# Performance work log

Measured on AMD Instinct MI355X. Metric: run time of the kernel, lower is better.

The kernel has to match this reference:

```python
import jax, jax.numpy as jnp
import numpy as np


def median_pool8(x):
    # x: (N, 1, H0, W0); 8x8 non-overlapping blocks, lower median (torch.median semantics)
    N, C, H0, W0 = x.shape
    H, W = H0 // 8, W0 // 8
    blocks = x.reshape(N, C, H, 8, W, 8).transpose(0, 1, 2, 4, 3, 5).reshape(N, C, H, W, 64)
    return jnp.sort(blocks, axis=-1)[..., (64 - 1) // 2]


def prelu(x, a):
    return jnp.where(x >= 0, x, a * x)


def setup_inputs() -> dict:
    key = jax.random.key(0)
    ks = jax.random.split(key, 12)
    N, C, H, W = 8, 128, 45, 60
    s = 0.05
    return {
        "cnn_encoder_output": jax.random.normal(ks[0], (N, C, H, W), jnp.float32),
        "original_input": jax.random.uniform(ks[1], (N, 4, H * 8, W * 8), jnp.float32),
        "xy": jax.random.normal(ks[2], (N, 2, H * 8, W * 8), jnp.float32),
        # g MLP: two Linear(128,128) + PReLU (single alpha each)
        "g_w0": jax.random.normal(ks[3], (C, C), jnp.float32) * s,
        "g_b0": jnp.zeros((C,), jnp.float32),
        "g_a0": jnp.full((1,), 0.25, jnp.float32),
        "g_w1": jax.random.normal(ks[4], (C, C), jnp.float32) * s,
        "g_b1": jnp.zeros((C,), jnp.float32),
        "g_a1": jnp.full((1,), 0.25, jnp.float32),
        # q update: Linear(256,128) + PReLU
        "q_w": jax.random.normal(ks[5], (C, 2 * C), jnp.float32) * s,
        "q_b": jnp.zeros((C,), jnp.float32),
        "q_a": jnp.full((1,), 0.25, jnp.float32),
        # output conv: Conv2d(256, 128, 3, padding=1)
        "conv_w": jax.random.normal(ks[6], (C, 2 * C, 3, 3), jnp.float32) * s,
        "conv_b": jnp.zeros((C,), jnp.float32),
        "gnn_iterations": 2,
        "k": 16,
        "use_half_precision": 0,
    }


def reference(cnn_encoder_output, original_input, xy,
              g_w0, g_b0, g_a0, g_w1, g_b1, g_a1,
              q_w, q_b, q_a, conv_w, conv_b,
              gnn_iterations, k, use_half_precision):
    N, C, H, W = cnn_encoder_output.shape
    HW = H * W

    # 3D projection: median-pooled x, y, depth -> (N, HW, 3)
    depth = median_pool8(original_input[:, 3:4])
    xc = median_pool8(xy[:, 0:1])
    yc = median_pool8(xy[:, 1:2])
    proj = jnp.concatenate([xc, yc, depth], axis=1).reshape(N, 3, HW).transpose(0, 2, 1)

    # batched KNN: D_ij = sqrt(|pi|^2 + |pj|^2 - 2 pi.pj), k smallest per row
    sq = jnp.sum(proj * proj, axis=-1)                        # (N, HW)
    r = jnp.einsum('nic,njc->nij', proj, proj)                # (N, HW, HW)
    D = jnp.sqrt(jnp.maximum(sq[:, :, None] + sq[:, None, :] - 2.0 * r, 0.0))
    _, knn = jax.lax.top_k(-D, k)                             # (N, HW, K) indices

    h = cnn_encoder_output.transpose(0, 2, 3, 1).reshape(N, HW, C)
    g_params = [(g_w0, g_b0, g_a0), (g_w1, g_b1, g_a1)]

    for _ in range(gnn_iterations):
        # gather neighbor features: (N, HW, K, C)
        nf = jax.vmap(lambda hn, kn: hn[kn])(h, knn)
        for w, b, a in g_params:
            nf = prelu(nf @ w.T + b, a)
        m = jnp.mean(nf, axis=2)                              # (N, HW, C)
        h = prelu(jnp.concatenate([h, m], axis=-1) @ q_w.T + q_b, q_a)

    h_img = h.reshape(N, H, W, C).transpose(0, 3, 1, 2)
    inp = jnp.concatenate([cnn_encoder_output, h_img], axis=1)  # (N, 2C, H, W)
    out = jax.lax.conv_general_dilated(
        inp, conv_w, window_strides=(1, 1), padding=((1, 1), (1, 1)),
        dimension_numbers=('NCHW', 'OIHW', 'NCHW')) + conv_b[None, :, None, None]
    return out
```

## Files before the change

### kernel.cpp

```cpp
#include <hip/hip_runtime.h>
#include <cfloat>
#include <cmath>

#define NB 8
#define CC 128
#define HH 45
#define WW 60
#define HWP 2700
#define KNN 16
#define H0 360
#define W0 480
#define NT 43
#define MROWS 21600

typedef __bf16 bf16_8 __attribute__((ext_vector_type(8)));
typedef __bf16 bf16_4 __attribute__((ext_vector_type(4)));
typedef float  f32x4  __attribute__((ext_vector_type(4)));

template <int K>
__device__ __forceinline__ void wfrag_body(const float* __restrict__ Wt,
                                           __bf16* __restrict__ wf, int bx, int tid) {
    int t = bx * 256 + tid;
    int j = t & 7;
    int lane = (t >> 3) & 63;
    int nt = (t >> 9) & 7;
    int kc = t >> 12;
    int oc = nt * 16 + (lane & 15);
    int k = kc * 32 + (lane >> 4) * 8 + j;
    wf[t] = (__bf16)Wt[(size_t)oc * K + k];
}

__global__ void __launch_bounds__(256) setup_all(
    const float* __restrict__ cnn, const float* __restrict__ xy,
    const float* __restrict__ orig,
    const float* __restrict__ g_w0, const float* __restrict__ g_w1,
    const float* __restrict__ q_w, const float* __restrict__ conv_w,
    __bf16* __restrict__ cnn_b, __bf16* __restrict__ pad_in,
    float* __restrict__ proj,
    __bf16* __restrict__ g0f, __bf16* __restrict__ g1f,
    __bf16* __restrict__ qf, __bf16* __restrict__ w_frag) {
    int bx = blockIdx.x;
    int tid = threadIdx.x;
    if (bx < 2720) {
        __shared__ float tile[32][33];
        int n = bx / 340;
        int r2 = bx % 340;
        int c0 = (r2 / 85) * 32;
        int p0 = (r2 % 85) * 32;
        int tx = tid & 31, ty = tid >> 5;
        #pragma unroll
        for (int r = 0; r < 32; r += 8) {
            int c = c0 + ty + r, p = p0 + tx;
            tile[ty + r][tx] = (p < HWP) ? cnn[((size_t)n * CC + c) * HWP + p] : 0.f;
        }
        __syncthreads();
        #pragma unroll
        for (int r = 0; r < 32; r += 8) {
            int p = p0 + ty + r, c = c0 + tx;
            if (p < HWP) {
                __bf16 bv = (__bf16)tile[tx][ty + r];
                cnn_b[((size_t)n * HWP + p) * 128 + c] = bv;
                int y = p / WW, x = p % WW;
                pad_in[(((size_t)n * 47 + y + 1) * 68 + (x + 1)) * 256 + c] = bv;
            }
        }
    } else if (bx < 2720 + 16200) {
        int w = (bx - 2720) * 4 + (tid >> 6);
        int lane = tid & 63;
        int n = w / (3 * HWP);
        int rem = w % (3 * HWP);
        int c = rem / HWP;
        int b = rem % HWP;
        const float* src = (c < 2) ? (xy + ((size_t)n * 2 + c) * H0 * W0)
                                   : (orig + ((size_t)n * 4 + 3) * H0 * W0);
        int by = b / WW, bxp = b % WW;
        int r = lane >> 3, col = lane & 7;
        float v = src[(by * 8 + r) * W0 + bxp * 8 + col];
        #pragma unroll
        for (int k = 2; k <= 64; k <<= 1) {
            #pragma unroll
            for (int j2 = k >> 1; j2 >= 1; j2 >>= 1) {
                float p = __shfl_xor(v, j2, 64);
                bool dir = (lane & k) == 0;
                bool low = (lane & j2) == 0;
                v = (dir == low) ? fminf(v, p) : fmaxf(v, p);
            }
        }
        if (lane == 31) proj[(size_t)c * (NB * HWP) + (size_t)n * HWP + b] = v;
    } else if (bx < 2720 + 16200 + 1408) {
        int pb = bx - (2720 + 16200);
        if (pb < 64)        wfrag_body<128>(g_w0, g0f, pb, tid);
        else if (pb < 128)  wfrag_body<128>(g_w1, g1f, pb - 64, tid);
        else if (pb < 256)  wfrag_body<256>(q_w, qf, pb - 128, tid);
        else {
            int t = (pb - 256) * 256 + tid;
            int j = t & 7;
            int lane = (t >> 3) & 63;
            int ntile = (t >> 9) & 7;
            int icc = (t >> 12) & 7;
            int tap = t >> 15;
            int oc = ntile * 16 + (lane & 15);
            int ic = icc * 32 + (lane >> 4) * 8 + j;
            w_frag[t] = (__bf16)conv_w[((size_t)oc * 256 + ic) * 9 + tap];
        }
    } else {
        int t = (bx - (2720 + 16200 + 1408)) * 256 + tid;
        int cg = t & 31;
        int s = t >> 5;
        int cell = s % 496;
        int n = s / 496;
        int y, x;
        if (cell < 136) { y = (cell < 68) ? 0 : 46; x = cell % 68; }
        else {
            int rem = cell - 136;
            y = 1 + rem / 8;
            int k = rem % 8;
            x = (k == 0) ? 0 : (60 + k);
        }
        bf16_8 z = {};
        *(bf16_8*)&pad_in[(((size_t)n * 47 + y) * 68 + x) * 256 + cg * 8] = z;
    }
}

__global__ void __launch_bounds__(512, 6) knn_kernel(const float* __restrict__ proj,
                                                     int* __restrict__ knn) {
#pragma clang fp contract(off)
    __shared__ float4 pts[HWP];
    __shared__ int sbufj[8][64];
    __shared__ int scnt[8];
    int n = blockIdx.y;
    const float* px = proj + (size_t)n * HWP;
    const float* py = proj + (size_t)NB * HWP + (size_t)n * HWP;
    const float* pz = proj + (size_t)2 * NB * HWP + (size_t)n * HWP;
    for (int t = threadIdx.x; t < HWP; t += 512) {
        float x = px[t], y = py[t], z = pz[t];
        float4 p;
        p.x = x; p.y = y; p.z = z;
        p.w = (x * x + y * y) + z * z;
        pts[t] = p;
    }
    __syncthreads();

    int wave = threadIdx.x >> 6;
    int lane = threadIdx.x & 63;
    int i = blockIdx.x * 8 + wave;
    if (i >= HWP) return;
    float4 pi = pts[i];
    float xi = pi.x, yi = pi.y, zi = pi.z, sqi = pi.w;

    unsigned int sdp[22];
    float mn = FLT_MAX;
    #pragma unroll
    for (int t = 0; t < NT; ++t) {
        int j = lane + t * 64;
        unsigned int u = 0xFFFFu;
        if (j < HWP) {
            float4 pj = pts[j];
            float r = fmaf(zi, pj.z, fmaf(yi, pj.y, xi * pj.x));
            float s = (sqi + pj.w) - 2.0f * r;
            mn = fminf(mn, s);
            float sc = fmaxf(s, 0.f);
            u = (__float_as_uint(sc) + 0xFFFFu) >> 16;
        }
        if (t & 1) sdp[t >> 1] |= (u << 16);
        else       sdp[t >> 1] = u;
    }

    float v = mn;
    #pragma unroll
    for (int k = 2; k <= 64; k <<= 1) {
        #pragma unroll
        for (int j2 = k >> 1; j2 >= 1; j2 >>= 1) {
            float p = __shfl_xor(v, j2, 64);
            bool dir = (lane & k) == 0;
            bool low = (lane & j2) == 0;
            v = (dir == low) ? fminf(v, p) : fmaxf(v, p);
        }
    }
    float M_s = __shfl(v, 15, 64);
    float M_test = (M_s > 0.f) ? (M_s * 1.0000005f + 1e-37f) : 0.0f;
    float M_t2 = M_test * 1.009f;
    unsigned int M16 = __float_as_uint(M_t2) >> 16;

    if (lane == 0) scnt[wave] = 0;
    #pragma unroll
    for (int t = 0; t < NT; ++t) {
        unsigned int u = (t & 1) ? (sdp[t >> 1] >> 16) : (sdp[t >> 1] & 0xFFFFu);
        if (u <= M16) {
            int slot = atomicAdd(&scnt[wave], 1);
            if (slot < 64) sbufj[wave][slot] = lane + t * 64;
        }
    }
    int cnt = scnt[wave];

    int myj = 0;
    if (cnt >= KNN && cnt <= 64) {
        unsigned long long key = ~0ull;
        if (lane < cnt) {
            int j = sbufj[wave][lane];
            float4 pj = pts[j];
            float r = fmaf(zi, pj.z, fmaf(yi, pj.y, xi * pj.x));
            float s = (sqi + pj.w) - 2.0f * r;
            float d = sqrtf(fmaxf(s, 0.f));
            key = ((unsigned long long)__float_as_uint(d) << 32) | (unsigned int)j;
        }
        #pragma unroll
        for (int k = 2; k <= 64; k <<= 1) {
            #pragma unroll
            for (int j2 = k >> 1; j2 >= 1; j2 >>= 1) {
                unsigned long long p = __shfl_xor(key, j2, 64);
                bool dir = (lane & k) == 0;
                bool low = (lane & j2) == 0;
                bool keepmin = (dir == low);
                bool pless = p < key;
                key = (pless == keepmin) ? p : key;
            }
        }
        myj = (int)(unsigned int)(key & 0xffffffffull);
    } else {
        float lastd = -FLT_MAX; int lastj = -1;
        #pragma unroll 1
        for (int r = 0; r < KNN; ++r) {
            float bd = FLT_MAX; int bj = 0x7fffffff;
            #pragma unroll 1
            for (int t = 0; t < NT; ++t) {
                int j = lane + t * 64;
                if (j < HWP) {
                    float4 pj = pts[j];
                    float rr = fmaf(zi, pj.z, fmaf(yi, pj.y, xi * pj.x));
                    float s = (sqi + pj.w) - 2.0f * rr;
                    float d = sqrtf(fmaxf(s, 0.f));
                    bool gt = (d > lastd) || (d == lastd && j > lastj);
                    bool lt = (d < bd) || (d == bd && j < bj);
                    if (gt && lt) { bd = d; bj = j; }
                }
            }
            float md = bd; int mj = bj;
            #pragma unroll
            for (int off = 32; off >= 1; off >>= 1) {
                float od = __shfl_xor(md, off, 64);
                int oj = __shfl_xor(mj, off, 64);
                if (od < md || (od == md && oj < mj)) { md = od; mj = oj; }
            }
            if (lane == r) myj = mj;
            lastd = md; lastj = mj;
        }
    }
    if (lane < KNN)
        knn[((size_t)n * HWP + i) * KNN + lane] = myj;
}

__device__ __forceinline__ void layer_b(
    const __bf16* __restrict__ src,
    const __bf16* __restrict__ wf,
    int wave, int lane, int kc_base, f32x4 acc[2][2]) {
    int quad = lane >> 4, lm = lane & 15;
    const bf16_8* wf8 = (const bf16_8*)wf;
    #pragma unroll
    for (int kc = 0; kc < 4; ++kc) {
        bf16_8 b[2], a[2];
        #pragma unroll
        for (int nt = 0; nt < 2; ++nt)
            b[nt] = *(const bf16_8*)&src[(nt * 16 + lm) * 136 + kc * 32 + quad * 8];
        #pragma unroll
        for (int mt = 0; mt < 2; ++mt)
            a[mt] = wf8[((size_t)(kc_base + kc) * 8 + (wave * 2 + mt)) * 64 + lane];
        #pragma unroll
        for (int mt = 0; mt < 2; ++mt)
            #pragma unroll
            for (int nt = 0; nt < 2; ++nt)
                acc[mt][nt] = __builtin_amdgcn_mfma_f32_16x16x32_bf16(
                    a[mt], b[nt], acc[mt][nt], 0, 0, 0);
    }
}

__global__ void __launch_bounds__(256) fused_g(
    const __bf16* __restrict__ Ain,
    const __bf16* __restrict__ w0f, const float* __restrict__ b0, const float* __restrict__ a0p,
    const __bf16* __restrict__ w1f, const float* __restrict__ b1, const float* __restrict__ a1p,
    __bf16* __restrict__ tgb) {
    __shared__ __bf16 albuf[32 * 136];
    __shared__ __bf16 inter[32 * 136];
    int bx = blockIdx.x;
    int nimg = bx & 7;
    int r0 = (bx >> 3) * 32;
    size_t base = (size_t)nimg * HWP;
    int tid = threadIdx.x;
    int wave = tid >> 6, lane = tid & 63;
    int quad = lane >> 4, lm = lane & 15;
    #pragma unroll
    for (int t = tid; t < 512; t += 256) {
        int row = t >> 4, c8 = (t & 15) * 8;
        int gr = r0 + row; if (gr >= HWP) gr = HWP - 1;
        *(bf16_8*)&albuf[row * 136 + c8] =
            *(const bf16_8*)&Ain[(base + gr) * 128 + c8];
    }
    __syncthreads();
    {
        f32x4 acc[2][2] = {};
        layer_b(albuf, w0f, wave, lane, 0, acc);
        float alpha = a0p[0];
        #pragma unroll
        for (int mt = 0; mt < 2; ++mt) {
            int oc0 = wave * 32 + mt * 16 + quad * 4;
            float4 bb = *(const float4*)&b0[oc0];
            float bv[4] = {bb.x, bb.y, bb.z, bb.w};
            #pragma unroll
            for (int nt = 0; nt < 2; ++nt) {
                bf16_4 o;
                #pragma unroll
                for (int reg = 0; reg < 4; ++reg) {
                    float vv = acc[mt][nt][reg] + bv[reg];
                    vv = (vv >= 0.f) ? vv : alpha * vv;
                    o[reg] = (__bf16)vv;
                }
                *(bf16_4*)&inter[(nt * 16 + lm) * 136 + oc0] = o;
            }
        }
    }
    __syncthreads();
    {
        f32x4 acc[2][2] = {};
        layer_b(inter, w1f, wave, lane, 0, acc);
        float alpha = a1p[0];
        #pragma unroll
        for (int mt = 0; mt < 2; ++mt) {
            int oc0 = wave * 32 + mt * 16 + quad * 4;
            float4 bb = *(const float4*)&b1[oc0];
            float bv[4] = {bb.x, bb.y, bb.z, bb.w};
            #pragma unroll
            for (int nt = 0; nt < 2; ++nt) {
                bf16_4 o;
                #pragma unroll
                for (int reg = 0; reg < 4; ++reg) {
                    float vv = acc[mt][nt][reg] + bv[reg];
                    vv = (vv >= 0.f) ? vv : alpha * vv;
                    o[reg] = (__bf16)vv;
                }
                int grow = r0 + nt * 16 + lm;
                if (grow < HWP)
                    *(bf16_4*)&tgb[(base + grow) * 128 + oc0] = o;
            }
        }
    }
}

__global__ void __launch_bounds__(256) fused_q(
    const __bf16* __restrict__ Ain, const __bf16* __restrict__ tgb,
    const int* __restrict__ knn_idx,
    const __bf16* __restrict__ qf, const float* __restrict__ qb,
    const float* __restrict__ qap,
    __bf16* __restrict__ out_lin, __bf16* __restrict__ pad_out, int mode) {
    __shared__ __bf16 hlds[32 * 136];
    __shared__ __bf16 mlds[32 * 136];
    int bx = blockIdx.x;
    int nimg = bx & 7;
    int r0 = (bx >> 3) * 32;
    size_t base = (size_t)nimg * HWP;
    int tid = threadIdx.x;
    int wave = tid >> 6, lane = tid & 63;
    int quad = lane >> 4, lm = lane & 15;
    #pragma unroll
    for (int t = tid; t < 512; t += 256) {
        int row = t >> 4, c8 = (t & 15) * 8;
        int gr = r0 + row; if (gr >= HWP) gr = HWP - 1;
        *(bf16_8*)&hlds[row * 136 + c8] =
            *(const bf16_8*)&Ain[(base + gr) * 128 + c8];
    }
    {
        int pix = tid >> 3;
        int oct0 = (tid & 7) * 2;
        int grow = r0 + pix; if (grow >= HWP) grow = HWP - 1;
        const int* kn = knn_idx + (base + grow) * KNN;
        const __bf16* tbase = tgb + base * 128;
        float a0[8] = {}, a1[8] = {};
        #pragma unroll
        for (int k = 0; k < KNN; ++k) {
            int j = kn[k];
            const __bf16* srcp = tbase + (size_t)j * 128 + oct0 * 8;
            bf16_8 v0 = *(const bf16_8*)srcp;
            bf16_8 v1 = *(const bf16_8*)(srcp + 8);
            #pragma unroll
            for (int e = 0; e < 8; ++e) { a0[e] += (float)v0[e]; a1[e] += (float)v1[e]; }
        }
        const float s = 1.f / 16.f;
        bf16_8 o0, o1;
        #pragma unroll
        for (int e = 0; e < 8; ++e) { o0[e] = (__bf16)(a0[e] * s); o1[e] = (__bf16)(a1[e] * s); }
        *(bf16_8*)&mlds[pix * 136 + oct0 * 8] = o0;
        *(bf16_8*)&mlds[pix * 136 + oct0 * 8 + 8] = o1;
    }
    __syncthreads();
    f32x4 acc[2][2] = {};
    layer_b(hlds, qf, wave, lane, 0, acc);
    layer_b(mlds, qf, wave, lane, 4, acc);
    float alpha = qap[0];
    #pragma unroll
    for (int mt = 0; mt < 2; ++mt) {
        int oc0 = wave * 32 + mt * 16 + quad * 4;
        float4 bb = *(const float4*)&qb[oc0];
        float bv[4] = {bb.x, bb.y, bb.z, bb.w};
        #pragma unroll
        for (int nt = 0; nt < 2; ++nt) {
            bf16_4 o;
            #pragma unroll
            for (int reg = 0; reg < 4; ++reg) {
                float vv = acc[mt][nt][reg] + bv[reg];
                vv = (vv >= 0.f) ? vv : alpha * vv;
                o[reg] = (__bf16)vv;
            }
            int grow = r0 + nt * 16 + lm;
            if (grow < HWP) {
                if (mode == 0) {
                    *(bf16_4*)&out_lin[(base + grow) * 128 + oc0] = o;
                } else {
                    int y = grow / WW, x = grow % WW;
                    *(bf16_4*)&pad_out[(((size_t)nimg * 47 + y + 1) * 68 + (x + 1)) * 256 + 128 + oc0] = o;
                }
            }
        }
    }
}

__global__ void __launch_bounds__(256) conv_mfma(
    const __bf16* __restrict__ pad_in,
    const __bf16* __restrict__ w_frag,
    const float* __restrict__ bias,
    float* __restrict__ out) {
    __shared__ __bf16 alds[3 * 66 * 72];
    int bx = blockIdx.x;
    int n = bx & 7;
    int rest = bx >> 3;
    int y = rest % HH;
    int oh = rest / HH;
    int tid = threadIdx.x;
    int wave = tid >> 6, lane = tid & 63;
    int wm = wave & 1, wq = wave >> 1;
    int quad = lane >> 4, lm = lane & 15;

    f32x4 acc[2][2] = {};
    const bf16_8* wf = (const bf16_8*)w_frag;

    for (int c64 = 0; c64 < 4; ++c64) {
        __syncthreads();
        for (int t = tid; t < 1584; t += 256) {
            int cq = t & 7;
            int xp = (t >> 3) % 66;
            int dy = (t >> 3) / 66;
            size_t src = (((size_t)n * 47 + (y + dy)) * 68 + xp) * 256 + c64 * 64 + cq * 8;
            *(bf16_8*)&alds[(dy * 66 + xp) * 72 + cq * 8] = *(const bf16_8*)&pad_in[src];
        }
        __syncthreads();
        #pragma unroll
        for (int tap = 0; tap < 9; ++tap) {
            int ky = tap / 3, kx = tap % 3;
            #pragma unroll
            for (int h = 0; h < 2; ++h) {
                int icc = c64 * 2 + h;
                bf16_8 b[2], a[2];
                #pragma unroll
                for (int nt = 0; nt < 2; ++nt)
                    b[nt] = wf[(((tap * 8 + icc) * 8) + (oh * 4 + wq * 2 + nt)) * 64 + lane];
                #pragma unroll
                for (int mt = 0; mt < 2; ++mt)
                    a[mt] = *(const bf16_8*)&alds[(ky * 66 + (wm * 32 + mt * 16 + lm + kx)) * 72
                                                  + h * 32 + quad * 8];
                #pragma unroll
                for (int mt = 0; mt < 2; ++mt)
                    #pragma unroll
                    for (int nt = 0; nt < 2; ++nt)
                        acc[mt][nt] = __builtin_amdgcn_mfma_f32_16x16x32_bf16(
                            a[mt], b[nt], acc[mt][nt], 0, 0, 0);
            }
        }
    }
    #pragma unroll
    for (int mt = 0; mt < 2; ++mt) {
        int x0 = wm * 32 + mt * 16 + quad * 4;
        if (x0 >= WW) continue;
        #pragma unroll
        for (int nt = 0; nt < 2; ++nt) {
            int oc = (oh * 4 + wq * 2 + nt) * 16 + lm;
            float bb = bias[oc];
            f32x4 v = acc[mt][nt];
            v[0] += bb; v[1] += bb; v[2] += bb; v[3] += bb;
            *(f32x4*)&out[(((size_t)n * 128 + oc) * HH + y) * WW + x0] = v;
        }
    }
}

extern "C" void kernel_launch(void* const* d_in, const int* in_sizes, int n_in,
                              void* d_out, int out_size, void* d_ws, size_t ws_size,
                              hipStream_t stream) {
    const float* cnn    = (const float*)d_in[0];
    const float* orig   = (const float*)d_in[1];
    const float* xy     = (const float*)d_in[2];
    const float* g_w0   = (const float*)d_in[3];
    const float* g_b0   = (const float*)d_in[4];
    const float* g_a0   = (const float*)d_in[5];
    const float* g_w1   = (const float*)d_in[6];
    const float* g_b1   = (const float*)d_in[7];
    const float* g_a1   = (const float*)d_in[8];
    const float* q_w    = (const float*)d_in[9];
    const float* q_b    = (const float*)d_in[10];
    const float* q_a    = (const float*)d_in[11];
    const float* conv_w = (const float*)d_in[12];
    const float* conv_b = (const float*)d_in[13];
    float* out = (float*)d_out;

    float* ws = (float*)d_ws;
    const size_t SB = (size_t)MROWS * 128;
    __bf16* cnn_b  = (__bf16*)ws;
    __bf16* h_b    = cnn_b + SB;
    __bf16* tgb    = h_b + SB;
    float*  proj   = (float*)(tgb + SB);
    int*    knn_i  = (int*)(proj + 64800);
    __bf16* g0f    = (__bf16*)(knn_i + (size_t)MROWS * KNN);
    __bf16* g1f    = g0f + 16384;
    __bf16* qf     = g1f + 16384;
    __bf16* w_frag = qf + 32768;
    __bf16* pad_in = w_frag + 294912;

    setup_all<<<2720 + 16200 + 1408 + 496, 256, 0, stream>>>(
        cnn, xy, orig, g_w0, g_w1, q_w, conv_w,
        cnn_b, pad_in, proj, g0f, g1f, qf, w_frag);
    knn_kernel<<<dim3(338, NB), 512, 0, stream>>>(proj, knn_i);

    fused_g<<<680, 256, 0, stream>>>(cnn_b, g0f, g_b0, g_a0, g1f, g_b1, g_a1, tgb);
    fused_q<<<680, 256, 0, stream>>>(cnn_b, tgb, knn_i, qf, q_b, q_a, h_b, pad_in, 0);

    fused_g<<<680, 256, 0, stream>>>(h_b, g0f, g_b0, g_a0, g1f, g_b1, g_a1, tgb);
    fused_q<<<680, 256, 0, stream>>>(h_b, tgb, knn_i, qf, q_b, q_a, h_b, pad_in, 1);

    conv_mfma<<<720, 256, 0, stream>>>(pad_in, w_frag, conv_b, out);
}
```

Baseline: 231.2 us.

## Fuse KNN with first g-MLP launch and merge q-update with next g-MLP

The KNN search and the first iteration's g MLP are independent, so they are merged into one launch. Block index selects either a KNN chunk or two 32-row g-MLP tiles sharing a raw shared-memory buffer. The first iteration's q update is fused with the second iteration's g MLP, reusing the freshly computed h tile from LDS and writing into a new tgb2 buffer. This cuts the launch count and overlaps the MFMA-light g work with the KNN blocks. The costs are a larger shared-memory footprint for the g blocks and an extra workspace region placed after pad_in.

```diff
diff --git a/kernel.cpp b/kernel.cpp
--- a/kernel.cpp
+++ b/kernel.cpp
@@ -122,134 +122,6 @@
     }
 }
 
-__global__ void __launch_bounds__(512, 6) knn_kernel(const float* __restrict__ proj,
-                                                     int* __restrict__ knn) {
-#pragma clang fp contract(off)
-    __shared__ float4 pts[HWP];
-    __shared__ int sbufj[8][64];
-    __shared__ int scnt[8];
-    int n = blockIdx.y;
-    const float* px = proj + (size_t)n * HWP;
-    const float* py = proj + (size_t)NB * HWP + (size_t)n * HWP;
-    const float* pz = proj + (size_t)2 * NB * HWP + (size_t)n * HWP;
-    for (int t = threadIdx.x; t < HWP; t += 512) {
-        float x = px[t], y = py[t], z = pz[t];
-        float4 p;
-        p.x = x; p.y = y; p.z = z;
-        p.w = (x * x + y * y) + z * z;
-        pts[t] = p;
-    }
-    __syncthreads();
-
-    int wave = threadIdx.x >> 6;
-    int lane = threadIdx.x & 63;
-    int i = blockIdx.x * 8 + wave;
-    if (i >= HWP) return;
-    float4 pi = pts[i];
-    float xi = pi.x, yi = pi.y, zi = pi.z, sqi = pi.w;
-
-    unsigned int sdp[22];
-    float mn = FLT_MAX;
-    #pragma unroll
-    for (int t = 0; t < NT; ++t) {
-        int j = lane + t * 64;
-        unsigned int u = 0xFFFFu;
-        if (j < HWP) {
-            float4 pj = pts[j];
-            float r = fmaf(zi, pj.z, fmaf(yi, pj.y, xi * pj.x));
-            float s = (sqi + pj.w) - 2.0f * r;
-            mn = fminf(mn, s);
-            float sc = fmaxf(s, 0.f);
-            u = (__float_as_uint(sc) + 0xFFFFu) >> 16;
-        }
-        if (t & 1) sdp[t >> 1] |= (u << 16);
-        else       sdp[t >> 1] = u;
-    }
-
-    float v = mn;
-    #pragma unroll
-    for (int k = 2; k <= 64; k <<= 1) {
-        #pragma unroll
-        for (int j2 = k >> 1; j2 >= 1; j2 >>= 1) {
-            float p = __shfl_xor(v, j2, 64);
-            bool dir = (lane & k) == 0;
-            bool low = (lane & j2) == 0;
-            v = (dir == low) ? fminf(v, p) : fmaxf(v, p);
-        }
-    }
-    float M_s = __shfl(v, 15, 64);
-    float M_test = (M_s > 0.f) ? (M_s * 1.0000005f + 1e-37f) : 0.0f;
-    float M_t2 = M_test * 1.009f;
-    unsigned int M16 = __float_as_uint(M_t2) >> 16;
-
-    if (lane == 0) scnt[wave] = 0;
-    #pragma unroll
-    for (int t = 0; t < NT; ++t) {
-        unsigned int u = (t & 1) ? (sdp[t >> 1] >> 16) : (sdp[t >> 1] & 0xFFFFu);
-        if (u <= M16) {
-            int slot = atomicAdd(&scnt[wave], 1);
-            if (slot < 64) sbufj[wave][slot] = lane + t * 64;
-        }
-    }
-    int cnt = scnt[wave];
-
-    int myj = 0;
-    if (cnt >= KNN && cnt <= 64) {
-        unsigned long long key = ~0ull;
-        if (lane < cnt) {
-            int j = sbufj[wave][lane];
-            float4 pj = pts[j];
-            float r = fmaf(zi, pj.z, fmaf(yi, pj.y, xi * pj.x));
-            float s = (sqi + pj.w) - 2.0f * r;
-            float d = sqrtf(fmaxf(s, 0.f));
-            key = ((unsigned long long)__float_as_uint(d) << 32) | (unsigned int)j;
-        }
-        #pragma unroll
-        for (int k = 2; k <= 64; k <<= 1) {
-            #pragma unroll
-            for (int j2 = k >> 1; j2 >= 1; j2 >>= 1) {
-                unsigned long long p = __shfl_xor(key, j2, 64);
-                bool dir = (lane & k) == 0;
-                bool low = (lane & j2) == 0;
-                bool keepmin = (dir == low);
-                bool pless = p < key;
-                key = (pless == keepmin) ? p : key;
-            }
-        }
-        myj = (int)(unsigned int)(key & 0xffffffffull);
-    } else {
-        float lastd = -FLT_MAX; int lastj = -1;
-        #pragma unroll 1
-        for (int r = 0; r < KNN; ++r) {
-            float bd = FLT_MAX; int bj = 0x7fffffff;
-            #pragma unroll 1
-            for (int t = 0; t < NT; ++t) {
-                int j = lane + t * 64;
-                if (j < HWP) {
-                    float4 pj = pts[j];
-                    float rr = fmaf(zi, pj.z, fmaf(yi, pj.y, xi * pj.x));
-                    float s = (sqi + pj.w) - 2.0f * rr;
-                    float d = sqrtf(fmaxf(s, 0.f));
-                    bool gt = (d > lastd) || (d == lastd && j > lastj);
-                    bool lt = (d < bd) || (d == bd && j < bj);
-                    if (gt && lt) { bd = d; bj = j; }
-                }
-            }
-            float md = bd; int mj = bj;
-            #pragma unroll
-            for (int off = 32; off >= 1; off >>= 1) {
-                float od = __shfl_xor(md, off, 64);
-                int oj = __shfl_xor(mj, off, 64);
-                if (od < md || (od == md && oj < mj)) { md = od; mj = oj; }
-            }
-            if (lane == r) myj = mj;
-            lastd = md; lastj = mj;
-        }
-    }
-    if (lane < KNN)
-        knn[((size_t)n * HWP + i) * KNN + lane] = myj;
-}
-
 __device__ __forceinline__ void layer_b(
     const __bf16* __restrict__ src,
     const __bf16* __restrict__ wf,
@@ -274,13 +146,221 @@
     }
 }
 
-__global__ void __launch_bounds__(256) fused_g(
+#define GBLK 340
+__global__ void __launch_bounds__(512, 6) knn_g1(
+    const float* __restrict__ proj, int* __restrict__ knn,
     const __bf16* __restrict__ Ain,
     const __bf16* __restrict__ w0f, const float* __restrict__ b0, const float* __restrict__ a0p,
     const __bf16* __restrict__ w1f, const float* __restrict__ b1, const float* __restrict__ a1p,
     __bf16* __restrict__ tgb) {
-    __shared__ __bf16 albuf[32 * 136];
-    __shared__ __bf16 inter[32 * 136];
+    __shared__ __align__(16) char smraw[45280];
+    int bx = blockIdx.x;
+    if (bx >= GBLK) {
+#pragma clang fp contract(off)
+        float4* pts = (float4*)smraw;
+        int (*sbufj)[64] = (int(*)[64])(smraw + 43200);
+        int* scnt = (int*)(smraw + 43200 + 2048);
+        int kb = bx - GBLK;
+        int n = kb & 7;
+        int chunk = kb >> 3;
+        const float* px = proj + (size_t)n * HWP;
+        const float* py = proj + (size_t)NB * HWP + (size_t)n * HWP;
+        const float* pz = proj + (size_t)2 * NB * HWP + (size_t)n * HWP;
+        for (int t = threadIdx.x; t < HWP; t += 512) {
+            float x = px[t], y = py[t], z = pz[t];
+            float4 p;
+            p.x = x; p.y = y; p.z = z;
+            p.w = (x * x + y * y) + z * z;
+            pts[t] = p;
+        }
+        __syncthreads();
+
+        int wave = threadIdx.x >> 6;
+        int lane = threadIdx.x & 63;
+        int i = chunk * 8 + wave;
+        if (i >= HWP) return;
+        float4 pi = pts[i];
+        float xi = pi.x, yi = pi.y, zi = pi.z, sqi = pi.w;
+
+        unsigned int sdp[22];
+        float mn = FLT_MAX;
+        #pragma unroll
+        for (int t = 0; t < NT; ++t) {
+            int j = lane + t * 64;
+            unsigned int u = 0xFFFFu;
+            if (j < HWP) {
+                float4 pj = pts[j];
+                float r = fmaf(zi, pj.z, fmaf(yi, pj.y, xi * pj.x));
+                float s = (sqi + pj.w) - 2.0f * r;
+                mn = fminf(mn, s);
+                float sc = fmaxf(s, 0.f);
+                u = (__float_as_uint(sc) + 0xFFFFu) >> 16;
+            }
+            if (t & 1) sdp[t >> 1] |= (u << 16);
+            else       sdp[t >> 1] = u;
+        }
+
+        float v = mn;
+        #pragma unroll
+        for (int k = 2; k <= 64; k <<= 1) {
+            #pragma unroll
+            for (int j2 = k >> 1; j2 >= 1; j2 >>= 1) {
+                float p = __shfl_xor(v, j2, 64);
+                bool dir = (lane & k) == 0;
+                bool low = (lane & j2) == 0;
+                v = (dir == low) ? fminf(v, p) : fmaxf(v, p);
+            }
+        }
+        float M_s = __shfl(v, 15, 64);
+        float M_test = (M_s > 0.f) ? (M_s * 1.0000005f + 1e-37f) : 0.0f;
+        float M_t2 = M_test * 1.009f;
+        unsigned int M16 = __float_as_uint(M_t2) >> 16;
+
+        if (lane == 0) scnt[wave] = 0;
+        #pragma unroll
+        for (int t = 0; t < NT; ++t) {
+            unsigned int u = (t & 1) ? (sdp[t >> 1] >> 16) : (sdp[t >> 1] & 0xFFFFu);
+            if (u <= M16) {
+                int slot = atomicAdd(&scnt[wave], 1);
+                if (slot < 64) sbufj[wave][slot] = lane + t * 64;
+            }
+        }
+        int cnt = scnt[wave];
+
+        int myj = 0;
+        if (cnt >= KNN && cnt <= 64) {
+            unsigned long long key = ~0ull;
+            if (lane < cnt) {
+                int j = sbufj[wave][lane];
+                float4 pj = pts[j];
+                float r = fmaf(zi, pj.z, fmaf(yi, pj.y, xi * pj.x));
+                float s = (sqi + pj.w) - 2.0f * r;
+                float d = sqrtf(fmaxf(s, 0.f));
+                key = ((unsigned long long)__float_as_uint(d) << 32) | (unsigned int)j;
+            }
+            #pragma unroll
+            for (int k = 2; k <= 64; k <<= 1) {
+                #pragma unroll
+                for (int j2 = k >> 1; j2 >= 1; j2 >>= 1) {
+                    unsigned long long p = __shfl_xor(key, j2, 64);
+                    bool dir = (lane & k) == 0;
+                    bool low = (lane & j2) == 0;
+                    bool keepmin = (dir == low);
+                    bool pless = p < key;
+                    key = (pless == keepmin) ? p : key;
+                }
+            }
+            myj = (int)(unsigned int)(key & 0xffffffffull);
+        } else {
+            float lastd = -FLT_MAX; int lastj = -1;
+            #pragma unroll 1
+            for (int r = 0; r < KNN; ++r) {
+                float bd = FLT_MAX; int bj = 0x7fffffff;
+                #pragma unroll 1
+                for (int t = 0; t < NT; ++t) {
+                    int j = lane + t * 64;
+                    if (j < HWP) {
+                        float4 pj = pts[j];
+                        float rr = fmaf(zi, pj.z, fmaf(yi, pj.y, xi * pj.x));
+                        float s = (sqi + pj.w) - 2.0f * rr;
+                        float d = sqrtf(fmaxf(s, 0.f));
+                        bool gt = (d > lastd) || (d == lastd && j > lastj);
+                        bool lt = (d < bd) || (d == bd && j < bj);
+                        if (gt && lt) { bd = d; bj = j; }
+                    }
+                }
+                float md = bd; int mj = bj;
+                #pragma unroll
+                for (int off = 32; off >= 1; off >>= 1) {
+                    float od = __shfl_xor(md, off, 64);
+                    int oj = __shfl_xor(mj, off, 64);
+                    if (od < md || (od == md && oj < mj)) { md = od; mj = oj; }
+                }
+                if (lane == r) myj = mj;
+                lastd = md; lastj = mj;
+            }
+        }
+        if (lane < KNN)
+            knn[((size_t)n * HWP + i) * KNN + lane] = myj;
+    } else {
+        int half = threadIdx.x >> 8;
+        int tid = threadIdx.x & 255;
+        int vb = bx * 2 + half;
+        __bf16* sb = (__bf16*)smraw;
+        __bf16* albuf = sb + half * (32 * 136);
+        __bf16* inter = sb + (2 + half) * (32 * 136);
+        int nimg = vb & 7;
+        int r0 = (vb >> 3) * 32;
+        size_t base = (size_t)nimg * HWP;
+        int wave = tid >> 6, lane = tid & 63;
+        int quad = lane >> 4, lm = lane & 15;
+        #pragma unroll
+        for (int t = tid; t < 512; t += 256) {
+            int row = t >> 4, c8 = (t & 15) * 8;
+            int gr = r0 + row; if (gr >= HWP) gr = HWP - 1;
+            *(bf16_8*)&albuf[row * 136 + c8] =
+                *(const bf16_8*)&Ain[(base + gr) * 128 + c8];
+        }
+        __syncthreads();
+        {
+            f32x4 acc[2][2] = {};
+            layer_b(albuf, w0f, wave, lane, 0, acc);
+            float alpha = a0p[0];
+            #pragma unroll
+            for (int mt = 0; mt < 2; ++mt) {
+                int oc0 = wave * 32 + mt * 16 + quad * 4;
+                float4 bb = *(const float4*)&b0[oc0];
+                float bv[4] = {bb.x, bb.y, bb.z, bb.w};
+                #pragma unroll
+                for (int nt = 0; nt < 2; ++nt) {
+                    bf16_4 o;
+                    #pragma unroll
+                    for (int reg = 0; reg < 4; ++reg) {
+                        float vv = acc[mt][nt][reg] + bv[reg];
+                        vv = (vv >= 0.f) ? vv : alpha * vv;
+                        o[reg] = (__bf16)vv;
+                    }
+                    *(bf16_4*)&inter[(nt * 16 + lm) * 136 + oc0] = o;
+                }
+            }
+        }
+        __syncthreads();
+        {
+            f32x4 acc[2][2] = {};
+            layer_b(inter, w1f, wave, lane, 0, acc);
+            float alpha = a1p[0];
+            #pragma unroll
+            for (int mt = 0; mt < 2; ++mt) {
+                int oc0 = wave * 32 + mt * 16 + quad * 4;
+                float4 bb = *(const float4*)&b1[oc0];
+                float bv[4] = {bb.x, bb.y, bb.z, bb.w};
+                #pragma unroll
+                for (int nt = 0; nt < 2; ++nt) {
+                    bf16_4 o;
+                    #pragma unroll
+                    for (int reg = 0; reg < 4; ++reg) {
+                        float vv = acc[mt][nt][reg] + bv[reg];
+                        vv = (vv >= 0.f) ? vv : alpha * vv;
+                        o[reg] = (__bf16)vv;
+                    }
+                    int grow = r0 + nt * 16 + lm;
+                    if (grow < HWP)
+                        *(bf16_4*)&tgb[(base + grow) * 128 + oc0] = o;
+                }
+            }
+        }
+    }
+}
+
+__global__ void __launch_bounds__(256) fused_qg(
+    const __bf16* __restrict__ Ain, const __bf16* __restrict__ tgb_in,
+    const int* __restrict__ knn_idx,
+    const __bf16* __restrict__ qf, const float* __restrict__ qb, const float* __restrict__ qap,
+    const __bf16* __restrict__ w0f, const float* __restrict__ b0, const float* __restrict__ a0p,
+    const __bf16* __restrict__ w1f, const float* __restrict__ b1, const float* __restrict__ a1p,
+    __bf16* __restrict__ h_out, __bf16* __restrict__ tgb_out) {
+    __shared__ __bf16 hlds[32 * 136];
+    __shared__ __bf16 mlds[32 * 136];
     int bx = blockIdx.x;
     int nimg = bx & 7;
     int r0 = (bx >> 3) * 32;
@@ -292,13 +372,64 @@
     for (int t = tid; t < 512; t += 256) {
         int row = t >> 4, c8 = (t & 15) * 8;
         int gr = r0 + row; if (gr >= HWP) gr = HWP - 1;
-        *(bf16_8*)&albuf[row * 136 + c8] =
+        *(bf16_8*)&hlds[row * 136 + c8] =
             *(const bf16_8*)&Ain[(base + gr) * 128 + c8];
+    }
+    {
+        int pix = tid >> 3;
+        int oct0 = (tid & 7) * 2;
+        int grow = r0 + pix; if (grow >= HWP) grow = HWP - 1;
+        const int* kn = knn_idx + (base + grow) * KNN;
+        const __bf16* tbase = tgb_in + base * 128;
+        float a0[8] = {}, a1[8] = {};
+        #pragma unroll
+        for (int k = 0; k < KNN; ++k) {
+            int j = kn[k];
+            const __bf16* srcp = tbase + (size_t)j * 128 + oct0 * 8;
+            bf16_8 v0 = *(const bf16_8*)srcp;
+            bf16_8 v1 = *(const bf16_8*)(srcp + 8);
+            #pragma unroll
+            for (int e = 0; e < 8; ++e) { a0[e] += (float)v0[e]; a1[e] += (float)v1[e]; }
+        }
+        const float s = 1.f / 16.f;
+        bf16_8 o0, o1;
+        #pragma unroll
+        for (int e = 0; e < 8; ++e) { o0[e] = (__bf16)(a0[e] * s); o1[e] = (__bf16)(a1[e] * s); }
+        *(bf16_8*)&mlds[pix * 136 + oct0 * 8] = o0;
+        *(bf16_8*)&mlds[pix * 136 + oct0 * 8 + 8] = o1;
     }
     __syncthreads();
     {
         f32x4 acc[2][2] = {};
-        layer_b(albuf, w0f, wave, lane, 0, acc);
+        layer_b(hlds, qf, wave, lane, 0, acc);
+        layer_b(mlds, qf, wave, lane, 4, acc);
+        __syncthreads();
+        float alpha = qap[0];
+        #pragma unroll
+        for (int mt = 0; mt < 2; ++mt) {
+            int oc0 = wave * 32 + mt * 16 + quad * 4;
+            float4 bb = *(const float4*)&qb[oc0];
+            float bv[4] = {bb.x, bb.y, bb.z, bb.w};
+            #pragma unroll
+            for (int nt = 0; nt < 2; ++nt) {
+                bf16_4 o;
+                #pragma unroll
+                for (int reg = 0; reg < 4; ++reg) {
+                    float vv = acc[mt][nt][reg] + bv[reg];
+                    vv = (vv >= 0.f) ? vv : alpha * vv;
+                    o[reg] = (__bf16)vv;
+                }
+                *(bf16_4*)&hlds[(nt * 16 + lm) * 136 + oc0] = o;
+                int grow = r0 + nt * 16 + lm;
+                if (grow < HWP)
+                    *(bf16_4*)&h_out[(base + grow) * 128 + oc0] = o;
+            }
+        }
+    }
+    __syncthreads();
+    {
+        f32x4 acc[2][2] = {};
+        layer_b(hlds, w0f, wave, lane, 0, acc);
         float alpha = a0p[0];
         #pragma unroll
         for (int mt = 0; mt < 2; ++mt) {
@@ -314,14 +445,14 @@
                     vv = (vv >= 0.f) ? vv : alpha * vv;
                     o[reg] = (__bf16)vv;
                 }
-                *(bf16_4*)&inter[(nt * 16 + lm) * 136 + oc0] = o;
+                *(bf16_4*)&mlds[(nt * 16 + lm) * 136 + oc0] = o;
             }
         }
     }
     __syncthreads();
     {
         f32x4 acc[2][2] = {};
-        layer_b(inter, w1f, wave, lane, 0, acc);
+        layer_b(mlds, w1f, wave, lane, 0, acc);
         float alpha = a1p[0];
         #pragma unroll
         for (int mt = 0; mt < 2; ++mt) {
@@ -339,7 +470,7 @@
                 }
                 int grow = r0 + nt * 16 + lm;
                 if (grow < HWP)
-                    *(bf16_4*)&tgb[(base + grow) * 128 + oc0] = o;
+                    *(bf16_4*)&tgb_out[(base + grow) * 128 + oc0] = o;
             }
         }
     }
@@ -520,17 +651,20 @@
     __bf16* qf     = g1f + 16384;
     __bf16* w_frag = qf + 32768;
     __bf16* pad_in = w_frag + 294912;
+    __bf16* tgb2   = pad_in + (size_t)NB * 47 * 68 * 256;
 
     setup_all<<<2720 + 16200 + 1408 + 496, 256, 0, stream>>>(
         cnn, xy, orig, g_w0, g_w1, q_w, conv_w,
         cnn_b, pad_in, proj, g0f, g1f, qf, w_frag);
-    knn_kernel<<<dim3(338, NB), 512, 0, stream>>>(proj, knn_i);
-
-    fused_g<<<680, 256, 0, stream>>>(cnn_b, g0f, g_b0, g_a0, g1f, g_b1, g_a1, tgb);
-    fused_q<<<680, 256, 0, stream>>>(cnn_b, tgb, knn_i, qf, q_b, q_a, h_b, pad_in, 0);
-
-    fused_g<<<680, 256, 0, stream>>>(h_b, g0f, g_b0, g_a0, g1f, g_b1, g_a1, tgb);
-    fused_q<<<680, 256, 0, stream>>>(h_b, tgb, knn_i, qf, q_b, q_a, h_b, pad_in, 1);
+
+    knn_g1<<<GBLK + 2704, 512, 0, stream>>>(
+        proj, knn_i, cnn_b, g0f, g_b0, g_a0, g1f, g_b1, g_a1, tgb);
+
+    fused_qg<<<680, 256, 0, stream>>>(
+        cnn_b, tgb, knn_i, qf, q_b, q_a,
+        g0f, g_b0, g_a0, g1f, g_b1, g_a1, h_b, tgb2);
+
+    fused_q<<<680, 256, 0, stream>>>(h_b, tgb2, knn_i, qf, q_b, q_a, h_b, pad_in, 1);
 
     conv_mfma<<<720, 256, 0, stream>>>(pad_in, w_frag, conv_b, out);
 }
```

Result: faster. 223.2 us (-3.5%).
